# Performance work log

Measured on AMD Instinct MI355X. Metric: run time of the kernel, lower is better.

Reference implementation:

```python
import jax, jax.numpy as jnp
import numpy as np

D = 256        # embedding_dim
N = 32768      # number of latent vectors (tokens)
K = 8192       # num_embeddings (codebook size)


def setup_inputs() -> dict:
    key = jax.random.key(0)
    k1, k2 = jax.random.split(key)
    z_e = jax.random.normal(k1, (D, N), dtype=jnp.float32)
    embeddings = jax.random.normal(k2, (K, D), dtype=jnp.float32)
    return {"z_e": z_e, "embeddings": embeddings}


def reference(z_e, embeddings):
    # z_e: (D, N), embeddings: (K, D)
    z = z_e.T  # (N, D)
    # squared euclidean distance via expansion ||z||^2 - 2 z.e + ||e||^2
    # (mathematically identical to sum((emb - z)**2, -1), avoids (N,K,D) temp)
    z_sq = jnp.sum(z * z, axis=1, keepdims=True)            # (N, 1)
    e_sq = jnp.sum(embeddings * embeddings, axis=1)         # (K,)
    dist = z_sq - 2.0 * (z @ embeddings.T) + e_sq[None, :]  # (N, K)
    indices = jnp.argmin(dist, axis=-1)                     # (N,)
    z_q = embeddings[indices].T                             # (D, N)
    return z_q, indices
```

## Files before the change

### kernel.cpp

```cpp
#include <hip/hip_runtime.h>

#define D_DIM 256
#define N_TOK 32768
#define K_CB  8192
#define TAU   0.12f
#define ZC_CAP 4096
#define SLABS 32
#define SLABW 256

typedef float    f32x16 __attribute__((ext_vector_type(16)));
typedef float    f32x4  __attribute__((ext_vector_type(4)));
typedef _Float16 f16x8  __attribute__((ext_vector_type(8)));

#define OFF_ESQ   0
#define OFF_CNT   32768
#define OFF_GDONE 33024
#define OFF_LIST  35072
#define OFF_FIXB  166144
#define OFF_EHT   524288
#define OFF_ZC    (OFF_EHT + 4194304)
#define MAXGRP    512
#define WS_NEED   ((size_t)(OFF_ZC + 4194304))

#define SMEM_MAIN 65536

__global__ __launch_bounds__(256) void eprep_kernel(const float* __restrict__ e,
                                                    short* __restrict__ eht,
                                                    float* __restrict__ esq,
                                                    int* __restrict__ cnt,
                                                    int* __restrict__ gdone) {
  __shared__ float ps[4 * 64];
  const int tid = threadIdx.x;
  const int kk = tid & 63, cc = tid >> 6;
  const int k = blockIdx.x * 64 + kk;
  if (blockIdx.x == 0) {
    if (tid == 0) *cnt = 0;
    if (tid < 256) { gdone[tid] = 0; gdone[tid + 256] = 0; }
  }
  _Float16* ef = (_Float16*)eht;
  float ss = 0.f;
  #pragma unroll
  for (int c2 = 0; c2 < 8; ++c2) {
    const int c = cc * 8 + c2;
    f32x4 v0 = *(const f32x4*)(e + (size_t)k * D_DIM + c * 8);
    f32x4 v1 = *(const f32x4*)(e + (size_t)k * D_DIM + c * 8 + 4);
    float v[8] = {v0[0], v0[1], v0[2], v0[3], v1[0], v1[1], v1[2], v1[3]};
    f16x8 hv;
    #pragma unroll
    for (int i = 0; i < 8; ++i) {
      ss += v[i] * v[i];
      hv[i] = (_Float16)v[i];
    }
    *(f16x8*)(ef + ((size_t)c * K_CB + k) * 8) = hv;
  }
  ps[cc * 64 + kk] = ss;
  __syncthreads();
  if (tid < 64)
    esq[blockIdx.x * 64 + tid] = ps[tid] + ps[64 + tid] + ps[128 + tid] + ps[192 + tid];
}

__global__ __launch_bounds__(1024, 4) void vq_main_kernel(
    const float* __restrict__ z, const float* __restrict__ e,
    const float* __restrict__ esq_g,
    const short* __restrict__ eht,
    float* __restrict__ out,
    int* __restrict__ cnt, int* __restrict__ list,
    unsigned long long* __restrict__ fixb, float* __restrict__ zc) {
  extern __shared__ char smem[];
  _Float16* zs = (_Float16*)smem;
  __shared__ int fin[128], slo[128];

  const int tid  = threadIdx.x;
  const int w    = tid >> 6;
  const int lane = tid & 63;
  const int half = lane >> 5;
  const int l31  = lane & 31;
  const int th   = w >> 3;
  const int cg   = w & 7;
  const int n0   = blockIdx.x * 128;
  const _Float16* ef = (const _Float16*)eht;

  {
    const int t  = tid & 127;
    const int cb = (tid >> 7) * 4;
    #pragma unroll
    for (int cc = 0; cc < 4; ++cc) {
      const int c = cb + cc;
      f16x8 hv;
      #pragma unroll
      for (int i = 0; i < 8; ++i)
        hv[i] = (_Float16)(-2.0f * z[(size_t)(c * 8 + i) * N_TOK + n0 + t]);
      *(f16x8*)(zs + ((size_t)c * 128 + t) * 8) = hv;
    }
  }
  __syncthreads();

  float bestv[2] = {3.4e38f, 3.4e38f};
  float secv[2]  = {3.4e38f, 3.4e38f};
  int   bestk[2] = {0, 0};

  for (int k0 = 0; k0 < K_CB; k0 += 512) {
    const int kb = k0 + cg * 64;

    f32x16 acc[2][2];
    #pragma unroll
    for (int f = 0; f < 2; ++f) {
      const int qb = kb + 32 * f + 4 * half;
      #pragma unroll
      for (int g = 0; g < 4; ++g) {
        f32x4 q = *(const f32x4*)(esq_g + qb + 8 * g);
        #pragma unroll
        for (int r = 0; r < 4; ++r) {
          const float qv = q[r];
          acc[f][0][g * 4 + r] = qv;
          acc[f][1][g * 4 + r] = qv;
        }
      }
    }

    #pragma unroll 2
    for (int dc = 0; dc < 16; ++dc) {
      f16x8 a[2], b[2];
      const size_t ebase = ((size_t)(2 * dc + half) * K_CB + kb + l31) * 8;
      a[0] = *(const f16x8*)(ef + ebase);
      a[1] = *(const f16x8*)(ef + ebase + 32 * 8);
      const int zb = ((2 * dc + half) * 128 + th * 64 + l31) * 8;
      b[0] = *(const f16x8*)(zs + zb);
      b[1] = *(const f16x8*)(zs + zb + 32 * 8);
      #pragma unroll
      for (int f = 0; f < 2; ++f)
        #pragma unroll
        for (int j = 0; j < 2; ++j)
          acc[f][j] = __builtin_amdgcn_mfma_f32_32x32x16_f16(a[f], b[j], acc[f][j], 0, 0, 0);
    }

    #pragma unroll
    for (int f = 0; f < 2; ++f) {
      const int base = kb + 32 * f + 4 * half;
      #pragma unroll
      for (int g = 0; g < 4; ++g) {
        #pragma unroll
        for (int r = 0; r < 4; ++r) {
          const int reg = g * 4 + r;
          const int kglob = base + 8 * g + r;
          #pragma unroll
          for (int j = 0; j < 2; ++j) {
            const float s = acc[f][j][reg];
            if (s < bestv[j]) { secv[j] = bestv[j]; bestv[j] = s; bestk[j] = kglob; }
            else if (s < secv[j]) secv[j] = s;
          }
        }
      }
    }
  }

  __syncthreads();
  float* pv  = (float*)(smem);
  int*   pk  = (int*)  (smem + 8192);
  float* ps2 = (float*)(smem + 16384);
  const int slot = cg * 2 + half;
  #pragma unroll
  for (int j = 0; j < 2; ++j) {
    const int t = th * 64 + j * 32 + l31;
    pv [slot * 128 + t] = bestv[j];
    pk [slot * 128 + t] = bestk[j];
    ps2[slot * 128 + t] = secv[j];
  }
  __syncthreads();
  if (tid < 128) {
    const int t = tid;
    float bv = pv[t]; int bk = pk[t]; float sc = ps2[t];
    #pragma unroll
    for (int s2 = 1; s2 < 16; ++s2) {
      float v = pv[s2 * 128 + t]; int k2 = pk[s2 * 128 + t]; float s3 = ps2[s2 * 128 + t];
      if (v < bv || (v == bv && k2 < bk)) { sc = fminf(bv, s3); bv = v; bk = k2; }
      else                                { sc = fminf(sc, v); }
    }
    fin[t] = bk;
    int sl = -1;
    const int n = n0 + t;
    out[(size_t)D_DIM * N_TOK + n] = (float)bk;
    if (sc - bv < TAU) {
      int p = atomicAdd(cnt, 1);
      list[p] = n;
      fixb[n] = 0xFFFFFFFFFFFFFFFFULL;
      if (p < ZC_CAP) sl = p;
    }
    slo[t] = sl;
  }
  __syncthreads();

  for (int tt = 0; tt < 128; ++tt) {
    const int p = slo[tt];
    if (p >= 0 && tid < 256)
      zc[(size_t)p * 256 + tid] = z[(size_t)tid * N_TOK + n0 + tt];
  }

  {
    const int t = tid & 127, d0 = tid >> 7;
    const int kk = fin[t];
    const f32x4* row = (const f32x4*)(e + (size_t)kk * D_DIM) + d0 * 8;
    #pragma unroll 4
    for (int q = 0; q < 8; ++q) {
      f32x4 v = row[q];
      const int d = d0 * 32 + q * 4;
      out[(size_t)(d + 0) * N_TOK + n0 + t] = v[0];
      out[(size_t)(d + 1) * N_TOK + n0 + t] = v[1];
      out[(size_t)(d + 2) * N_TOK + n0 + t] = v[2];
      out[(size_t)(d + 3) * N_TOK + n0 + t] = v[3];
    }
  }
}

__global__ __launch_bounds__(256) void rescan_kernel(
    const float* __restrict__ z, const float* __restrict__ zc,
    const float* __restrict__ e,
    const float* __restrict__ esq, const int* __restrict__ cnt,
    const int* __restrict__ list, unsigned long long* __restrict__ fixb,
    int* __restrict__ gdone, float* __restrict__ out) {
  __shared__ float zs[D_DIM * 64];
  __shared__ unsigned long long red[16 * 64];
  __shared__ int fk[64], fn[64], lastflag;
  const int tid = threadIdx.x;
  const int c = *(volatile const int*)cnt;
  if (c == 0) return;
  int groups = (c + 63) >> 6;
  if (groups > MAXGRP) groups = MAXGRP;
  const int items = groups * SLABS;
  const int tx = tid & 15, ty = tid >> 4;

  for (int it = blockIdx.x; it < items; it += gridDim.x) {
    const int g = it / SLABS;
    const int slab = (it % SLABS) * SLABW;
    __syncthreads();
    if (g < (ZC_CAP >> 6)) {
      const int t = tid & 63, seg = tid >> 6;
      const int idx = g * 64 + t;
      const float* src = zc + (size_t)(idx < c ? idx : c - 1) * 256 + seg * 64;
      #pragma unroll
      for (int r = 0; r < 16; ++r) {
        f32x4 v = *(const f32x4*)(src + r * 4);
        const int d = seg * 64 + r * 4;
        zs[(d + 0) * 64 + t] = v[0];
        zs[(d + 1) * 64 + t] = v[1];
        zs[(d + 2) * 64 + t] = v[2];
        zs[(d + 3) * 64 + t] = v[3];
      }
    } else {
      const int t = tid & 63, dq = tid >> 6;
      const int idx = g * 64 + t;
      const int n = list[idx < c ? idx : c - 1];
      #pragma unroll 4
      for (int dd = 0; dd < 64; ++dd) {
        const int d = dq * 64 + dd;
        zs[d * 64 + t] = z[(size_t)d * N_TOK + n];
      }
    }
    __syncthreads();

    unsigned long long lmin[4] = {~0ULL, ~0ULL, ~0ULL, ~0ULL};
    #pragma unroll
    for (int k0 = 0; k0 < SLABW; k0 += 64) {
      const f32x4* er[4]; float eqv[4];
      #pragma unroll
      for (int j = 0; j < 4; ++j) {
        int k = slab + k0 + ty + 16 * j;
        er[j] = (const f32x4*)(e + (size_t)k * D_DIM);
        eqv[j] = esq[k];
      }
      float acc[4][4];
      #pragma unroll
      for (int i = 0; i < 4; ++i)
        #pragma unroll
        for (int j = 0; j < 4; ++j) acc[i][j] = 0.f;
      #pragma unroll 4
      for (int d4 = 0; d4 < D_DIM / 4; ++d4) {
        f32x4 ev[4];
        #pragma unroll
        for (int j = 0; j < 4; ++j) ev[j] = er[j][d4];
        #pragma unroll
        for (int dd = 0; dd < 4; ++dd) {
          float zv[4];
          #pragma unroll
          for (int i = 0; i < 4; ++i) zv[i] = zs[(d4 * 4 + dd) * 64 + tx + 16 * i];
          #pragma unroll
          for (int i = 0; i < 4; ++i)
            #pragma unroll
            for (int j = 0; j < 4; ++j) acc[i][j] += zv[i] * ev[j][dd];
        }
      }
      #pragma unroll
      for (int j = 0; j < 4; ++j) {
        const int k = slab + k0 + ty + 16 * j;
        #pragma unroll
        for (int i = 0; i < 4; ++i) {
          float s = eqv[j] - 2.0f * acc[i][j] + 1024.0f;
          unsigned long long p =
              ((unsigned long long)__float_as_uint(s) << 32) | (unsigned)k;
          lmin[i] = (p < lmin[i]) ? p : lmin[i];
        }
      }
    }
    #pragma unroll
    for (int i = 0; i < 4; ++i) red[ty * 64 + tx + 16 * i] = lmin[i];
    __syncthreads();
    if (tid < 64) {
      unsigned long long m = red[tid];
      #pragma unroll
      for (int t = 1; t < 16; ++t) {
        unsigned long long v = red[t * 64 + tid];
        m = (v < m) ? v : m;
      }
      const int idx = g * 64 + tid;
      const int n = list[idx < c ? idx : c - 1];
      atomicMin(&fixb[n], m);
    }
    __threadfence();
    __syncthreads();
    if (tid == 0) lastflag = (atomicAdd(&gdone[g], 1) == SLABS - 1) ? 1 : 0;
    __syncthreads();
    if (lastflag) {
      if (tid < 64) {
        const int idx = g * 64 + tid;
        int kres = -1, n = -1;
        if (idx < c) {
          n = list[idx];
          unsigned long long mv = atomicMin(&fixb[n], 0xFFFFFFFFFFFFFFFFULL);
          kres = (int)(unsigned)(mv & 0xFFFFFFFFu);
          out[(size_t)D_DIM * N_TOK + n] = (float)kres;
        }
        fk[tid] = kres; fn[tid] = n;
      }
      __syncthreads();
      {
        const int t = tid & 63, dq = tid >> 6;
        const int kres = fk[t];
        if (kres >= 0) {
          const int n = fn[t];
          const float* row = e + (size_t)kres * D_DIM;
          #pragma unroll 4
          for (int dd = 0; dd < 64; ++dd) {
            const int d = dq * 64 + dd;
            out[(size_t)d * N_TOK + n] = row[d];
          }
        }
      }
    }
  }
}

__global__ __launch_bounds__(256) void esq_kernel(const float* __restrict__ e,
                                                  float* __restrict__ esq) {
  const int wave = threadIdx.x >> 6, lane = threadIdx.x & 63;
  const int k = blockIdx.x * 4 + wave;
  const float4* row = (const float4*)(e + (size_t)k * D_DIM);
  float4 v = row[lane];
  float s = v.x*v.x + v.y*v.y + v.z*v.z + v.w*v.w;
  #pragma unroll
  for (int off = 32; off > 0; off >>= 1) s += __shfl_down(s, off, 64);
  if (lane == 0) esq[k] = s;
}

__global__ __launch_bounds__(256) void vq_kernel(const float* __restrict__ z,
                                                 const float* __restrict__ e,
                                                 const float* __restrict__ esq,
                                                 float* __restrict__ out) {
  __shared__ float zs[D_DIM][64];
  const int tid = threadIdx.x, tx = tid & 15, ty = tid >> 4;
  const int n0 = blockIdx.x * 64;
  {
    const int c = tid & 63, d0 = tid >> 6;
    #pragma unroll 4
    for (int d = d0; d < D_DIM; d += 4) zs[d][c] = z[(size_t)d * N_TOK + n0 + c];
  }
  __syncthreads();
  float bestv[4] = {3.4e38f,3.4e38f,3.4e38f,3.4e38f};
  int   besti[4] = {0,0,0,0};
  for (int k0 = 0; k0 < K_CB; k0 += 64) {
    const float4* er[4]; float eqv[4];
    #pragma unroll
    for (int j = 0; j < 4; ++j) {
      int k = k0 + ty + 16 * j;
      er[j] = (const float4*)(e + (size_t)k * D_DIM);
      eqv[j] = esq[k];
    }
    float acc[4][4];
    #pragma unroll
    for (int i = 0; i < 4; ++i)
      #pragma unroll
      for (int j = 0; j < 4; ++j) acc[i][j] = 0.f;
    #pragma unroll 4
    for (int d4 = 0; d4 < D_DIM/4; ++d4) {
      float4 ev[4];
      #pragma unroll
      for (int j = 0; j < 4; ++j) ev[j] = er[j][d4];
      #pragma unroll
      for (int dd = 0; dd < 4; ++dd) {
        float zv[4];
        #pragma unroll
        for (int i = 0; i < 4; ++i) zv[i] = zs[d4*4+dd][tx + 16*i];
        #pragma unroll
        for (int i = 0; i < 4; ++i)
          #pragma unroll
          for (int j = 0; j < 4; ++j) acc[i][j] += zv[i] * ((const float*)&ev[j])[dd];
      }
    }
    #pragma unroll
    for (int j = 0; j < 4; ++j) {
      int k = k0 + ty + 16 * j;
      #pragma unroll
      for (int i = 0; i < 4; ++i) {
        float s = eqv[j] - 2.0f * acc[i][j];
        if (s < bestv[i]) { bestv[i] = s; besti[i] = k; }
      }
    }
  }
  __syncthreads();
  float* lds = &zs[0][0];
  float* vred = lds; int* ired = (int*)lds + 1024; int* fin = (int*)lds + 2048;
  #pragma unroll
  for (int i = 0; i < 4; ++i) {
    int l = tx + 16 * i;
    vred[ty * 64 + l] = bestv[i]; ired[ty * 64 + l] = besti[i];
  }
  __syncthreads();
  if (tid < 64) {
    float bv = vred[tid]; int bi = ired[tid];
    #pragma unroll
    for (int t = 1; t < 16; ++t) {
      float v = vred[t*64+tid]; int ix = ired[t*64+tid];
      if (v < bv || (v == bv && ix < bi)) { bv = v; bi = ix; }
    }
    fin[tid] = bi;
    out[(size_t)D_DIM * N_TOK + n0 + tid] = (float)bi;
  }
  __syncthreads();
  {
    const int l = tid & 63, d0 = tid >> 6;
    const int kk = fin[l];
    const float* row = e + (size_t)kk * D_DIM;
    #pragma unroll 4
    for (int d = d0; d < D_DIM; d += 4) out[(size_t)d * N_TOK + n0 + l] = row[d];
  }
}

extern "C" void kernel_launch(void* const* d_in, const int* in_sizes, int n_in,
                              void* d_out, int out_size, void* d_ws, size_t ws_size,
                              hipStream_t stream) {
  const float* z = (const float*)d_in[0];
  const float* e = (const float*)d_in[1];
  float* out = (float*)d_out;
  char* ws = (char*)d_ws;

  if (ws_size >= WS_NEED) {
    float* esq = (float*)(ws + OFF_ESQ);
    int* cnt = (int*)(ws + OFF_CNT);
    int* gdone = (int*)(ws + OFF_GDONE);
    int* list = (int*)(ws + OFF_LIST);
    unsigned long long* fixb = (unsigned long long*)(ws + OFF_FIXB);
    short* eht = (short*)(ws + OFF_EHT);
    float* zc = (float*)(ws + OFF_ZC);

    (void)hipFuncSetAttribute((const void*)vq_main_kernel,
                              hipFuncAttributeMaxDynamicSharedMemorySize, SMEM_MAIN);

    eprep_kernel<<<128, 256, 0, stream>>>(e, eht, esq, cnt, gdone);
    vq_main_kernel<<<256, 1024, SMEM_MAIN, stream>>>(z, e, esq, eht,
                                                     out, cnt, list, fixb, zc);
    rescan_kernel<<<512, 256, 0, stream>>>(z, zc, e, esq, cnt, list, fixb, gdone, out);
  } else {
    float* esq = (float*)(ws);
    esq_kernel<<<K_CB / 4, 256, 0, stream>>>(e, esq);
    vq_kernel<<<N_TOK / 64, 256, 0, stream>>>(z, e, esq, out);
  }
}
```

Baseline: 342.4 us.

## Double-buffer codebook tiles in LDS via async global_load_lds

Stages fp16 codebook tiles into a double-buffered LDS region using global_load_lds, prefetching the next tile while MFMAs consume the current one, so each workgroup's waves share one staged copy. The e_sq norms are also copied into LDS once rather than read from global memory on every tile. This raises LDS use to 160KB per block, which limits occupancy to one block per CU. It also adds a __syncthreads per 4-channel step, which may serialize the waves.

```diff
diff --git a/kernel.cpp b/kernel.cpp
--- a/kernel.cpp
+++ b/kernel.cpp
@@ -22,7 +22,11 @@
 #define MAXGRP    512
 #define WS_NEED   ((size_t)(OFF_ZC + 4194304))
 
-#define SMEM_MAIN 65536
+#define SMEM_MAIN 163840
+
+#define GLOAD_LDS16(g, s) \
+  __builtin_amdgcn_global_load_lds((const __attribute__((address_space(1))) unsigned int*)(g), \
+                                   (__attribute__((address_space(3))) unsigned int*)(s), 16, 0, 0)
 
 __global__ __launch_bounds__(256) void eprep_kernel(const float* __restrict__ e,
                                                     short* __restrict__ eht,
@@ -59,6 +63,18 @@
     esq[blockIdx.x * 64 + tid] = ps[tid] + ps[64 + tid] + ps[128 + tid] + ps[192 + tid];
 }
 
+static __device__ __forceinline__ void stage_etile(const _Float16* __restrict__ ef,
+                                                   char* esp, int c0, int k0,
+                                                   int w, int lane) {
+  #pragma unroll
+  for (int q = 0; q < 2; ++q) {
+    const int u = q * 1024 + w * 64 + lane;
+    const int chunk = u >> 9, off = u & 511;
+    GLOAD_LDS16(ef + ((size_t)(c0 + chunk) * K_CB + k0 + off) * 8,
+                (_Float16*)esp + (size_t)(q * 1024 + w * 64) * 8);
+  }
+}
+
 __global__ __launch_bounds__(1024, 4) void vq_main_kernel(
     const float* __restrict__ z, const float* __restrict__ e,
     const float* __restrict__ esq_g,
@@ -68,7 +84,7 @@
     unsigned long long* __restrict__ fixb, float* __restrict__ zc) {
   extern __shared__ char smem[];
   _Float16* zs = (_Float16*)smem;
-  __shared__ int fin[128], slo[128];
+  float* eqs   = (float*)(smem + 131072);
 
   const int tid  = threadIdx.x;
   const int w    = tid >> 6;
@@ -80,6 +96,13 @@
   const int n0   = blockIdx.x * 128;
   const _Float16* ef = (const _Float16*)eht;
 
+  #pragma unroll
+  for (int i = 0; i < 2; ++i) {
+    int idx = (w * 2 + i) * 256;
+    GLOAD_LDS16(esq_g + idx + lane * 4, eqs + idx);
+  }
+  stage_etile(ef, smem + 65536, 0, 0, w, lane);
+
   {
     const int t  = tid & 127;
     const int cb = (tid >> 7) * 4;
@@ -99,6 +122,7 @@
   float secv[2]  = {3.4e38f, 3.4e38f};
   int   bestk[2] = {0, 0};
 
+  int buf = 0;
   for (int k0 = 0; k0 < K_CB; k0 += 512) {
     const int kb = k0 + cg * 64;
 
@@ -108,30 +132,41 @@
       const int qb = kb + 32 * f + 4 * half;
       #pragma unroll
       for (int g = 0; g < 4; ++g) {
-        f32x4 q = *(const f32x4*)(esq_g + qb + 8 * g);
+        f32x4 q = *(const f32x4*)(eqs + qb + 8 * g);
         #pragma unroll
         for (int r = 0; r < 4; ++r) {
-          const float qv = q[r];
-          acc[f][0][g * 4 + r] = qv;
-          acc[f][1][g * 4 + r] = qv;
+          acc[f][0][g * 4 + r] = q[r];
+          acc[f][1][g * 4 + r] = q[r];
         }
       }
     }
 
-    #pragma unroll 2
-    for (int dc = 0; dc < 16; ++dc) {
-      f16x8 a[2], b[2];
-      const size_t ebase = ((size_t)(2 * dc + half) * K_CB + kb + l31) * 8;
-      a[0] = *(const f16x8*)(ef + ebase);
-      a[1] = *(const f16x8*)(ef + ebase + 32 * 8);
-      const int zb = ((2 * dc + half) * 128 + th * 64 + l31) * 8;
-      b[0] = *(const f16x8*)(zs + zb);
-      b[1] = *(const f16x8*)(zs + zb + 32 * 8);
-      #pragma unroll
-      for (int f = 0; f < 2; ++f)
-        #pragma unroll
-        for (int j = 0; j < 2; ++j)
-          acc[f][j] = __builtin_amdgcn_mfma_f32_32x32x16_f16(a[f], b[j], acc[f][j], 0, 0, 0);
+    #pragma unroll 1
+    for (int s = 0; s < 8; ++s) {
+      {
+        int nc = (s + 1) * 4, nk = k0;
+        if (s == 7) { nc = 0; nk = k0 + 512; }
+        if (nk < K_CB)
+          stage_etile(ef, smem + 65536 + ((buf ^ 1) << 15), nc, nk, w, lane);
+      }
+      const _Float16* eb = (const _Float16*)(smem + 65536 + (buf << 15));
+      #pragma unroll
+      for (int dcL = 0; dcL < 2; ++dcL) {
+        f16x8 a[2], b[2];
+        const int ar = ((2 * dcL + half) << 9) + cg * 64 + l31;
+        a[0] = *(const f16x8*)(eb + (size_t)ar * 8);
+        a[1] = *(const f16x8*)(eb + (size_t)(ar + 32) * 8);
+        const int cglob = s * 4 + 2 * dcL + half;
+        const int zb = (cglob * 128 + th * 64 + l31) * 8;
+        b[0] = *(const f16x8*)(zs + zb);
+        b[1] = *(const f16x8*)(zs + zb + 32 * 8);
+        acc[0][0] = __builtin_amdgcn_mfma_f32_32x32x16_f16(a[0], b[0], acc[0][0], 0, 0, 0);
+        acc[0][1] = __builtin_amdgcn_mfma_f32_32x32x16_f16(a[0], b[1], acc[0][1], 0, 0, 0);
+        acc[1][0] = __builtin_amdgcn_mfma_f32_32x32x16_f16(a[1], b[0], acc[1][0], 0, 0, 0);
+        acc[1][1] = __builtin_amdgcn_mfma_f32_32x32x16_f16(a[1], b[1], acc[1][1], 0, 0, 0);
+      }
+      __syncthreads();
+      buf ^= 1;
     }
 
     #pragma unroll
@@ -158,6 +193,8 @@
   float* pv  = (float*)(smem);
   int*   pk  = (int*)  (smem + 8192);
   float* ps2 = (float*)(smem + 16384);
+  int*   fin = (int*)  (smem + 24576);
+  int*   slo = (int*)  (smem + 25088);
   const int slot = cg * 2 + half;
   #pragma unroll
   for (int j = 0; j < 2; ++j) {
```

Result: faster. 334.3 us (-2.4%).
